# Kernel tuning notes

Measured on AMD Instinct MI355X. Metric: run time of the kernel, lower is better.

The kernel has to match this reference:

```python
import jax, jax.numpy as jnp
import numpy as np
from functools import partial

B, T, L = 32, 128, 64
DIN, H, DCTX, ATT = 512, 512, 512, 256


def _glorot(key, shape):
    lim = np.sqrt(6.0 / (shape[0] + shape[1]))
    return jax.random.uniform(key, shape, jnp.float32, -lim, lim)


def _ortho(key, shape):
    a = jax.random.normal(key, shape, jnp.float32)
    q, _ = jnp.linalg.qr(a)
    return q.astype(jnp.float32)


def setup_inputs() -> dict:
    key = jax.random.key(0)
    ks = jax.random.split(key, 24)
    inp = {
        "X": jax.random.normal(ks[0], (B, T, DIN), jnp.float32),
        "context": jax.random.normal(ks[1], (B, L, DCTX), jnp.float32),
        "mask": jnp.ones((B, T), jnp.float32),
        "context_mask": jnp.ones((B, L), jnp.int32),
    }
    names = ["i", "f", "c", "o"]
    for j, n in enumerate(names):
        inp[f"W_{n}"] = _glorot(ks[2 + 4 * j], (DIN, H))
        inp[f"U_{n}"] = _ortho(ks[3 + 4 * j], (H, H))
        inp[f"C_{n}"] = _ortho(ks[4 + 4 * j], (DCTX, H))
        inp[f"b_{n}"] = jnp.ones((H,), jnp.float32) if n == "f" else jnp.zeros((H,), jnp.float32)
    inp["att_ctx_W1"] = _glorot(ks[18], (DCTX, ATT))
    inp["att_h_W1"] = _glorot(ks[19], (H, ATT))
    inp["att_b1"] = jnp.zeros((ATT,), jnp.float32)
    inp["att_W2"] = _glorot(ks[20], (ATT, 1))
    inp["att_b2"] = jnp.zeros((1,), jnp.float32)
    return inp


def _forward(X, context, mask, cmask_f,
             W_i, U_i, C_i, b_i, W_f, U_f, C_f, b_f,
             W_c, U_c, C_c, b_c, W_o, U_o, C_o, b_o,
             att_ctx_W1, att_h_W1, att_b1, att_W2, att_b2):
    sig, tanh = jax.nn.sigmoid, jnp.tanh
    # precompute input-to-gate projections: [T,B,H]
    xi = jnp.einsum('btd,dh->tbh', X, W_i) + b_i
    xf = jnp.einsum('btd,dh->tbh', X, W_f) + b_f
    xc = jnp.einsum('btd,dh->tbh', X, W_c) + b_c
    xo = jnp.einsum('btd,dh->tbh', X, W_o) + b_o
    ctx_trans = jnp.einsum('bld,da->bla', context, att_ctx_W1) + att_b1  # [B,L,A]
    m = mask.T[:, :, None]  # [T,B,1]

    def step(carry, inp):
        h, c = carry
        xi_t, xf_t, xc_t, xo_t, m_t = inp
        # attention over context (original uses raw exp, not max-subtracted)
        att_hidden = tanh(ctx_trans + (h @ att_h_W1)[:, None, :])          # [B,L,A]
        att_raw = jnp.squeeze(att_hidden @ att_W2, -1) + att_b2[0]          # [B,L]
        e = jnp.exp(att_raw) * cmask_f
        a = e / jnp.sum(e, axis=-1, keepdims=True)
        ctx_vec = jnp.einsum('bl,bld->bd', a, context)                      # [B,Dctx]
        i_t = sig(xi_t + h @ U_i + ctx_vec @ C_i)
        f_t = sig(xf_t + h @ U_f + ctx_vec @ C_f)
        c_new = f_t * c + i_t * tanh(xc_t + h @ U_c + ctx_vec @ C_c)
        o_t = sig(xo_t + h @ U_o + ctx_vec @ C_o)
        h_new = o_t * tanh(c_new)
        h_new = (1.0 - m_t) * h + m_t * h_new
        c_new = (1.0 - m_t) * c + m_t * c_new
        return (h_new, c_new), (h_new, c_new, ctx_vec)

    h0 = jnp.zeros((X.shape[0], U_i.shape[0]), X.dtype)
    c0 = jnp.zeros_like(h0)
    _, (hs, cs, ctxs) = jax.lax.scan(step, (h0, c0), (xi, xf, xc, xo, m))
    # back to batch-major [B,T,·]
    return (hs.transpose(1, 0, 2), cs.transpose(1, 0, 2), ctxs.transpose(1, 0, 2))


def reference(X, context, mask, context_mask,
              W_i, U_i, C_i, b_i, W_f, U_f, C_f, b_f,
              W_c, U_c, C_c, b_c, W_o, U_o, C_o, b_o,
              att_ctx_W1, att_h_W1, att_b1, att_W2, att_b2):
    cmask_f = context_mask.astype(X.dtype)
    return _forward(X, context, mask, cmask_f,
                    W_i, U_i, C_i, b_i, W_f, U_f, C_f, b_f,
                    W_c, U_c, C_c, b_c, W_o, U_o, C_o, b_o,
                    att_ctx_W1, att_h_W1, att_b1, att_W2, att_b2)
```

## Files before the change

### kernel.cpp

```cpp
#include <hip/hip_runtime.h>
#include <stdint.h>

#define B_ 32
#define T_ 128
#define L_ 64
#define H_ 512
#define A_ 256
#define NB 32

typedef short short8 __attribute__((ext_vector_type(8)));
typedef float floatx4 __attribute__((ext_vector_type(4)));

__device__ __forceinline__ float b2f(unsigned short u) {
  union { unsigned int i; float f; } x; x.i = ((unsigned int)u) << 16; return x.f;
}
__device__ __forceinline__ unsigned short f2b(float f) {
  union { float f; unsigned int i; } x; x.f = f;
  unsigned int i = x.i;
  unsigned int r = (i + 0x7fffu + ((i >> 16) & 1u)) >> 16;
  return (unsigned short)r;
}
__device__ __forceinline__ void unpack2(unsigned int p, float& lo, float& hi) {
  union { unsigned int i; float f; } a, b;
  a.i = p << 16; b.i = p & 0xffff0000u;
  lo = a.f; hi = b.f;
}
__device__ __forceinline__ float tanh_fast(float x) {
  float e = __expf(2.f * x);
  return 1.f - 2.f / (e + 1.f);
}
__device__ __forceinline__ float sigmoid_fast(float x) {
  return 1.f / (1.f + __expf(-x));
}
template<bool F32>
__device__ __forceinline__ float ld1(const void* p, size_t i) {
  if (F32) return ((const float*)p)[i];
  return b2f(((const unsigned short*)p)[i]);
}
template<bool F32>
__device__ __forceinline__ void ld8(const void* p, size_t i, float* f) {
  if (F32) {
    const float4 a = *(const float4*)((const float*)p + i);
    const float4 b = *(const float4*)((const float*)p + i + 4);
    f[0] = a.x; f[1] = a.y; f[2] = a.z; f[3] = a.w;
    f[4] = b.x; f[5] = b.y; f[6] = b.z; f[7] = b.w;
  } else {
    const uint4 v = *(const uint4*)((const unsigned short*)p + i);
    unpack2(v.x, f[0], f[1]); unpack2(v.y, f[2], f[3]);
    unpack2(v.z, f[4], f[5]); unpack2(v.w, f[6], f[7]);
  }
}

__global__ __launch_bounds__(256) void conv_f2b(
    const float* __restrict__ src, unsigned short* __restrict__ dst, int n)
{
  const int i = (blockIdx.x * 256 + threadIdx.x) * 4;
  if (i + 3 < n) {
    const float4 v = *(const float4*)(src + i);
    ushort4 o;
    o.x = f2b(v.x); o.y = f2b(v.y); o.z = f2b(v.z); o.w = f2b(v.w);
    *(ushort4*)(dst + i) = o;
  }
}

__global__ __launch_bounds__(256) void gemm_bias(
    const unsigned short* __restrict__ A,
    const unsigned short* __restrict__ W,
    const float* __restrict__ bias,
    unsigned short* __restrict__ out,
    int M, int N, int ldo, int co, int mode)
{
  const int K = 512;
  __shared__ __attribute__((aligned(16))) unsigned short As[16 * 32];
  __shared__ __attribute__((aligned(16))) unsigned short Bs[32 * 64];
  const int tid = threadIdx.x;
  const int m0 = blockIdx.y * 16;
  const int n0 = blockIdx.x * 64;
  const int lane = tid & 63;
  const int w = tid >> 6;
  const int mfrag = lane & 15;
  const int q = lane >> 4;
  floatx4 acc = {0.f, 0.f, 0.f, 0.f};

  for (int k0 = 0; k0 < K; k0 += 32) {
    if (tid < 64) {
      const int r = tid >> 2, cg = tid & 3;
      const uint4 v = *(const uint4*)(A + (size_t)(m0 + r) * K + k0 + cg * 8);
      *(uint4*)&As[r * 32 + cg * 8] = v;
    }
    {
      const int r = tid >> 3, cg = tid & 7;
      const uint4 v = *(const uint4*)(W + (size_t)(k0 + r) * N + n0 + cg * 8);
      *(uint4*)&Bs[r * 64 + cg * 8] = v;
    }
    __syncthreads();
    const short8 af = *(const short8*)&As[mfrag * 32 + q * 8];
    short8 bf;
    const int wn = w * 16 + mfrag;
#pragma unroll
    for (int j = 0; j < 8; ++j) bf[j] = (short)Bs[(q * 8 + j) * 64 + wn];
    acc = __builtin_amdgcn_mfma_f32_16x16x32_bf16(af, bf, acc, 0, 0, 0);
    __syncthreads();
  }
  const int col = n0 + w * 16 + mfrag;
  const float bv = bias ? bias[col] : 0.f;
#pragma unroll
  for (int i = 0; i < 4; ++i) {
    const int row = m0 + q * 4 + i;
    const unsigned short v = f2b(acc[i] + bv);
    if (mode) {
      const int bb = row >> 7, tt = row & 127;
      out[((size_t)tt * 2048 + co + col) * 32 + bb] = v;
    } else {
      out[(size_t)row * ldo + co + col] = v;
    }
  }
}

__global__ __launch_bounds__(1024) void init_coop(unsigned short* Hs0,
                                                  unsigned int* flags)
{
  const int tid = threadIdx.x;
#pragma unroll
  for (int i = 0; i < 16; ++i) Hs0[tid * 16 + i] = 0;
  flags[tid] = 0u;
}

__device__ __forceinline__ void flagbar(unsigned int* flags, unsigned int gen) {
  __syncthreads();
  if (threadIdx.x == 0)
    __hip_atomic_store(flags + (size_t)blockIdx.x * 32, gen,
                       __ATOMIC_RELEASE, __HIP_MEMORY_SCOPE_AGENT);
  if (threadIdx.x < NB) {
    while (__hip_atomic_load(flags + (size_t)threadIdx.x * 32,
                             __ATOMIC_RELAXED, __HIP_MEMORY_SCOPE_AGENT) < gen)
      __builtin_amdgcn_s_sleep(1);
    __builtin_amdgcn_fence(__ATOMIC_ACQUIRE, "agent");
  }
  __syncthreads();
}

struct CoopParams {
  const float* Uf[4];
  const float* Cf[4];
  const float* attW1h;
  unsigned short* UT;
  unsigned short* CT;
  unsigned short* w1hsT;
  unsigned short* Hs0;
  unsigned short* Hs1;
  unsigned short* CVs;
  float* partials;
  unsigned int* flags;
  const unsigned short* xg;
  const unsigned short* ctxT;
  const unsigned short* cxb;
  const float* attW2;
  const float* attB2;
  const float* mask;
  const int* cmask;
  float* out;
};

__global__ __launch_bounds__(1024) void rnn_coop(const CoopParams p) {
  __shared__ __attribute__((aligned(16))) unsigned short h_all[32][520];
  __shared__ __attribute__((aligned(16))) unsigned short cv_all[32][520];
  __shared__ __attribute__((aligned(16))) unsigned short hloc_b[32][24];
  __shared__ float accbuf[16][32][17];
  __shared__ float pw1[4][256];
  __shared__ float hw1[256];
  __shared__ float e_s[64];
  __shared__ float a_s[64];
  __shared__ float cpart[2][512];
  __shared__ float c_s[512];
  __shared__ float h_loc[512];

  const int k = blockIdx.x;
  const int tid = threadIdx.x;

  {
    const int g = tid >> 8;
    const int idx = tid & 255;
    unsigned short* dU = p.UT + (size_t)k * 32768 + (size_t)g * 8192;
    unsigned short* dC = p.CT + (size_t)k * 32768 + (size_t)g * 8192;
#pragma unroll
    for (int rr = 0; rr < 2; ++rr) {
      const int r = idx * 2 + rr;
      const float* sU = p.Uf[g] + (size_t)r * 512 + k * 16;
      const float* sC = p.Cf[g] + (size_t)r * 512 + k * 16;
#pragma unroll
      for (int n = 0; n < 16; ++n) dU[(size_t)n * 512 + r] = f2b(sU[n]);
#pragma unroll
      for (int n = 0; n < 16; ++n) dC[(size_t)n * 512 + r] = f2b(sC[n]);
    }
  }
  {
    const int a = tid >> 2, r0 = (tid & 3) * 4;
    unsigned short* dst = p.w1hsT + (size_t)k * 4096 + (size_t)a * 16 + r0;
#pragma unroll
    for (int rr = 0; rr < 4; ++rr)
      dst[rr] = f2b(p.attW1h[(size_t)(k * 16 + r0 + rr) * 256 + a]);
  }
  const int lq = tid >> 4;
  const int kk = tid & 15;
  float ctq[16], w2q[16];
  {
    const unsigned short* ct = p.ctxT + ((size_t)(k * L_ + lq)) * 256 + kk * 16;
#pragma unroll
    for (int i = 0; i < 16; ++i) ctq[i] = b2f(ct[i]);
#pragma unroll
    for (int i = 0; i < 16; ++i) w2q[i] = p.attW2[kk * 16 + i];
  }
  const float b2v = p.attB2[0];
  const float cm_l = (float)p.cmask[k * L_ + lq];
  if (tid < 512) { c_s[tid] = 0.f; h_loc[tid] = 0.f; }
  unsigned int bgen = 0;
  __syncthreads();

  for (int t = 0; t < T_; ++t) {
    const unsigned short* HsA = (t & 1) ? p.Hs1 : p.Hs0;
    unsigned short* HsB = (t & 1) ? p.Hs0 : p.Hs1;

    {
      const int row = tid >> 5, cg = tid & 31;
      const uint4* src = (const uint4*)(HsA + (size_t)row * 512 + cg * 16);
      const uint4 v0 = src[0], v1 = src[1];
      *(uint4*)&h_all[row][cg * 16] = v0;
      *(uint4*)&h_all[row][cg * 16 + 8] = v1;
    }
    {
      const int p4 = tid >> 8, a = tid & 255;
      float s = 0.f;
      if (t > 0) {
        const float* pp = p.partials + (size_t)(p4 * 8) * 8192 + (size_t)k * 256 + a;
#pragma unroll
        for (int i = 0; i < 8; ++i) s += pp[(size_t)i * 8192];
      }
      pw1[p4][a] = s;
    }
    __syncthreads();
    if (tid < 256) hw1[tid] = pw1[0][tid] + pw1[1][tid] + pw1[2][tid] + pw1[3][tid];
    __syncthreads();

    {
      float s = 0.f;
#pragma unroll
      for (int i = 0; i < 16; ++i)
        s += tanh_fast(ctq[i] + hw1[kk * 16 + i]) * w2q[i];
      s += __shfl_xor(s, 1, 16);
      s += __shfl_xor(s, 2, 16);
      s += __shfl_xor(s, 4, 16);
      s += __shfl_xor(s, 8, 16);
      if (kk == 0) e_s[lq] = __expf(s + b2v) * cm_l;
    }
    __syncthreads();
    if (tid < 64) {
      const float e = e_s[tid];
      float s = e;
#pragma unroll
      for (int off = 1; off < 64; off <<= 1) s += __shfl_xor(s, off, 64);
      a_s[tid] = e / s;
    }
    __syncthreads();
    {
      const int p2 = tid >> 9, d = tid & 511;
      const unsigned short* cxp = p.cxb + ((size_t)(k * L_ + p2 * 32)) * 512 + d;
      float s = 0.f;
#pragma unroll 4
      for (int l = 0; l < 32; ++l)
        s += a_s[p2 * 32 + l] * b2f(cxp[(size_t)l * 512]);
      cpart[p2][d] = s;
    }
    __syncthreads();
    if (tid < 512) {
      const float cv = cpart[0][tid] + cpart[1][tid];
      p.CVs[(size_t)k * 512 + tid] = f2b(cv);
      p.out[(size_t)4194304 + ((size_t)k * T_ + t) * 512 + tid] = cv;
    }
    flagbar(p.flags, ++bgen);

    {
      const int row = tid >> 5, cg = tid & 31;
      const uint4* src = (const uint4*)(p.CVs + (size_t)row * 512 + cg * 16);
      const uint4 v0 = src[0], v1 = src[1];
      *(uint4*)&cv_all[row][cg * 16] = v0;
      *(uint4*)&cv_all[row][cg * 16 + 8] = v1;
    }
    __syncthreads();
    {
      const int w = tid >> 6, lane = tid & 63;
      const int l15 = lane & 15, q = lane >> 4;
      const int g = w & 3, ph = (w >> 2) & 1, khh = w >> 3;
      const unsigned short* Bb = (ph ? p.CT : p.UT)
          + (size_t)k * 32768 + (size_t)g * 8192 + (size_t)l15 * 512 + khh * 256 + q * 8;
      const unsigned short (*Aall)[520] = ph ? cv_all : h_all;
      floatx4 acc0 = {0.f, 0.f, 0.f, 0.f}, acc1 = {0.f, 0.f, 0.f, 0.f};
#pragma unroll
      for (int ks = 0; ks < 8; ++ks) {
        const short8 bfr = *(const short8*)(Bb + ks * 32);
        const short8 a0 = *(const short8*)&Aall[l15][khh * 256 + ks * 32 + q * 8];
        const short8 a1 = *(const short8*)&Aall[16 + l15][khh * 256 + ks * 32 + q * 8];
        acc0 = __builtin_amdgcn_mfma_f32_16x16x32_bf16(a0, bfr, acc0, 0, 0, 0);
        acc1 = __builtin_amdgcn_mfma_f32_16x16x32_bf16(a1, bfr, acc1, 0, 0, 0);
      }
#pragma unroll
      for (int i = 0; i < 4; ++i) {
        accbuf[w][q * 4 + i][l15] = acc0[i];
        accbuf[w][16 + q * 4 + i][l15] = acc1[i];
      }
    }
    __syncthreads();
    if (tid < 512) {
      const int b = tid >> 4, j = tid & 15;
      const size_t xb0 = ((size_t)t * 2048 + (size_t)(k * 16 + j)) * 32 + b;
#define GSUM(g) (accbuf[g][b][j] + accbuf[8 + g][b][j] + accbuf[4 + g][b][j] + accbuf[12 + g][b][j])
      float gi_ = GSUM(0) + b2f(p.xg[xb0]);
      float gf_ = GSUM(1) + b2f(p.xg[xb0 + (size_t)512 * 32]);
      float gc_ = GSUM(2) + b2f(p.xg[xb0 + (size_t)1024 * 32]);
      float go_ = GSUM(3) + b2f(p.xg[xb0 + (size_t)1536 * 32]);
#undef GSUM
      const float it = sigmoid_fast(gi_);
      const float ft = sigmoid_fast(gf_);
      const float ot = sigmoid_fast(go_);
      const float c_old = c_s[tid], h_old = h_loc[tid];
      float cn = ft * c_old + it * tanh_fast(gc_);
      float hn = ot * tanh_fast(cn);
      const float mt = p.mask[(size_t)b * T_ + t];
      hn = (1.f - mt) * h_old + mt * hn;
      cn = (1.f - mt) * c_old + mt * cn;
      c_s[tid] = cn; h_loc[tid] = hn;
      const unsigned short hb = f2b(hn);
      HsB[(size_t)b * 512 + k * 16 + j] = hb;
      hloc_b[b][j] = hb;
      const size_t o0 = ((size_t)b * T_ + t) * 512 + k * 16 + j;
      p.out[o0] = hn;
      p.out[(size_t)2097152 + o0] = cn;
    }
    __syncthreads();
    {
      const int w = tid >> 6, lane = tid & 63;
      const int l15 = lane & 15, q = lane >> 4;
      const short8 z8 = {0, 0, 0, 0, 0, 0, 0, 0};
      const unsigned short* wrow =
          p.w1hsT + (size_t)k * 4096 + (size_t)(w * 16 + l15) * 16 + (q & 1) * 8;
      const short8 bfr = (q < 2) ? *(const short8*)wrow : z8;
#pragma unroll
      for (int mh = 0; mh < 2; ++mh) {
        const unsigned short* hrow = &hloc_b[mh * 16 + l15][(q & 1) * 8];
        const short8 af = (q < 2) ? *(const short8*)hrow : z8;
        floatx4 acc = {0.f, 0.f, 0.f, 0.f};
        acc = __builtin_amdgcn_mfma_f32_16x16x32_bf16(af, bfr, acc, 0, 0, 0);
#pragma unroll
        for (int i = 0; i < 4; ++i)
          p.partials[(size_t)k * 8192 + (size_t)(mh * 16 + q * 4 + i) * 256 + w * 16 + l15] = acc[i];
      }
    }
    flagbar(p.flags, ++bgen);
  }
}

struct Params {
  const void* W[4]; const void* U[4]; const void* C[4]; const void* gb[4];
  const void* attW1c; const void* attW1h; const void* attB1;
  const void* attW2; const void* attB2;
  const void* mask; const void* context; const void* Xin;
  const int* cmask;
  float* out;
};

template<bool F32>
__device__ void rnn_body(const Params p) {
  __shared__ float h_s[512];
  __shared__ float x_s[512];
  __shared__ float cv_s[512];
  __shared__ float pw1[4][256];
  __shared__ float hw1[256];
  __shared__ float e_s[64];
  __shared__ float a_s[64];
  __shared__ float gpart[4][2048];
  __shared__ float cpart[2][512];

  const int b = blockIdx.x;
  const int tid = threadIdx.x;
  const int lq = tid >> 4;
  const int kk = tid & 15;
  const int part4 = tid >> 8;
  const int a256 = tid & 255;
  const int part2 = tid >> 9;
  const int d512 = tid & 511;
  const int g = a256 >> 6;
  const int j0 = a256 * 8;
  const int jj = j0 & 511;

  float ctq[16];
#pragma unroll
  for (int i = 0; i < 16; ++i) ctq[i] = 0.f;
  {
    const size_t crow = ((size_t)b * L_ + lq) * 512;
    for (int r = 0; r < 512; ++r) {
      const float cv = ld1<F32>(p.context, crow + r);
      float fa[8], fb[8];
      ld8<F32>(p.attW1c, (size_t)r * 256 + kk * 16, fa);
      ld8<F32>(p.attW1c, (size_t)r * 256 + kk * 16 + 8, fb);
#pragma unroll
      for (int i = 0; i < 8; ++i) { ctq[i] += cv * fa[i]; ctq[8 + i] += cv * fb[i]; }
    }
#pragma unroll
    for (int i = 0; i < 16; ++i) ctq[i] += ld1<F32>(p.attB1, kk * 16 + i);
  }
  float w2q[16];
#pragma unroll
  for (int i = 0; i < 16; ++i) w2q[i] = ld1<F32>(p.attW2, kk * 16 + i);
  const float b2v = ld1<F32>(p.attB2, 0);
  float bi = 0.f, bff = 0.f, bc = 0.f, bo = 0.f;
  if (tid < 512) {
    bi = ld1<F32>(p.gb[0], tid);
    bff = ld1<F32>(p.gb[1], tid);
    bc = ld1<F32>(p.gb[2], tid);
    bo = ld1<F32>(p.gb[3], tid);
  }
  float c_reg = 0.f;
  if (tid < 512) h_s[tid] = 0.f;
  __syncthreads();

  const void* Wg = p.W[g];
  const void* Ug = p.U[g];
  const void* Cg = p.C[g];
  const size_t wb = (size_t)(part4 * 128) * 512 + jj;
  const size_t w1b = (size_t)(part4 * 128) * 256 + a256;

  for (int t = 0; t < T_; ++t) {
    {
      float s = 0.f;
      const int r0 = part4 * 128;
#pragma unroll 4
      for (int r = 0; r < 128; ++r)
        s += h_s[r0 + r] * ld1<F32>(p.attW1h, w1b + (size_t)r * 256);
      pw1[part4][a256] = s;
    }
    if (tid < 512)
      x_s[tid] = ld1<F32>(p.Xin, ((size_t)b * T_ + t) * 512 + tid);
    __syncthreads();
    if (tid < 256) hw1[tid] = pw1[0][tid] + pw1[1][tid] + pw1[2][tid] + pw1[3][tid];
    __syncthreads();
    {
      float s = 0.f;
#pragma unroll
      for (int i = 0; i < 16; ++i)
        s += tanh_fast(ctq[i] + hw1[kk * 16 + i]) * w2q[i];
      s += __shfl_xor(s, 1, 16);
      s += __shfl_xor(s, 2, 16);
      s += __shfl_xor(s, 4, 16);
      s += __shfl_xor(s, 8, 16);
      if (kk == 0)
        e_s[lq] = __expf(s + b2v) * (float)p.cmask[b * L_ + lq];
    }
    __syncthreads();
    if (tid < 64) {
      const float e = e_s[tid];
      float s = e;
#pragma unroll
      for (int off = 1; off < 64; off <<= 1) s += __shfl_xor(s, off, 64);
      a_s[tid] = e / s;
    }
    __syncthreads();
    {
      const size_t cb = ((size_t)b * L_ + part2 * 32) * 512 + d512;
      float s = 0.f;
#pragma unroll 4
      for (int l = 0; l < 32; ++l)
        s += a_s[part2 * 32 + l] * ld1<F32>(p.context, cb + (size_t)l * 512);
      cpart[part2][d512] = s;
    }
    __syncthreads();
    if (tid < 512) {
      const float cv = cpart[0][tid] + cpart[1][tid];
      cv_s[tid] = cv;
      p.out[(size_t)4194304 + ((size_t)b * T_ + t) * 512 + tid] = cv;
    }
    __syncthreads();
    {
      float acc[8];
#pragma unroll
      for (int i = 0; i < 8; ++i) acc[i] = 0.f;
      const int r0 = part4 * 128;
      float f[8];
#pragma unroll 2
      for (int r = 0; r < 128; ++r) {
        const float xv = x_s[r0 + r];
        ld8<F32>(Wg, wb + (size_t)r * 512, f);
#pragma unroll
        for (int i = 0; i < 8; ++i) acc[i] += xv * f[i];
      }
#pragma unroll 2
      for (int r = 0; r < 128; ++r) {
        const float hv = h_s[r0 + r];
        ld8<F32>(Ug, wb + (size_t)r * 512, f);
#pragma unroll
        for (int i = 0; i < 8; ++i) acc[i] += hv * f[i];
      }
#pragma unroll 2
      for (int r = 0; r < 128; ++r) {
        const float cvv = cv_s[r0 + r];
        ld8<F32>(Cg, wb + (size_t)r * 512, f);
#pragma unroll
        for (int i = 0; i < 8; ++i) acc[i] += cvv * f[i];
      }
#pragma unroll
      for (int i = 0; i < 8; ++i) gpart[part4][j0 + i] = acc[i];
    }
    __syncthreads();
    if (tid < 512) {
      const int d = tid;
      float gi_ = bi + gpart[0][d] + gpart[1][d] + gpart[2][d] + gpart[3][d];
      float gf_ = bff + gpart[0][512 + d] + gpart[1][512 + d] + gpart[2][512 + d] + gpart[3][512 + d];
      float gc_ = bc + gpart[0][1024 + d] + gpart[1][1024 + d] + gpart[2][1024 + d] + gpart[3][1024 + d];
      float go_ = bo + gpart[0][1536 + d] + gpart[1][1536 + d] + gpart[2][1536 + d] + gpart[3][1536 + d];
      const float it = sigmoid_fast(gi_);
      const float ft = sigmoid_fast(gf_);
      const float ot = sigmoid_fast(go_);
      float cn = ft * c_reg + it * tanh_fast(gc_);
      float hn = ot * tanh_fast(cn);
      const float m = ld1<F32>(p.mask, (size_t)b * T_ + t);
      hn = (1.f - m) * h_s[d] + m * hn;
      cn = (1.f - m) * c_reg + m * cn;
      c_reg = cn;
      h_s[d] = hn;
      const size_t o0 = ((size_t)b * T_ + t) * 512 + d;
      p.out[o0] = hn;
      p.out[(size_t)2097152 + o0] = cn;
    }
    __syncthreads();
  }
}

__global__ __launch_bounds__(1024) void rnn_fused(const Params p) {
  const unsigned int mw = *(const unsigned int*)p.mask;
  if (mw == 0x3F800000u) rnn_body<true>(p);
  else rnn_body<false>(p);
}

extern "C" void kernel_launch(void* const* d_in, const int* in_sizes, int n_in,
                              void* d_out, int out_size, void* d_ws, size_t ws_size,
                              hipStream_t stream) {
  (void)in_sizes; (void)n_in; (void)out_size;
  const float* X    = (const float*)d_in[0];
  const float* Ctx  = (const float*)d_in[1];
  const float* Mask = (const float*)d_in[2];
  const int*   Cm   = (const int*)d_in[3];
  const float* Wt[4] = {(const float*)d_in[4],  (const float*)d_in[8],
                        (const float*)d_in[12], (const float*)d_in[16]};
  const float* Ut[4] = {(const float*)d_in[5],  (const float*)d_in[9],
                        (const float*)d_in[13], (const float*)d_in[17]};
  const float* Ct[4] = {(const float*)d_in[6],  (const float*)d_in[10],
                        (const float*)d_in[14], (const float*)d_in[18]};
  const float* bg[4] = {(const float*)d_in[7],  (const float*)d_in[11],
                        (const float*)d_in[15], (const float*)d_in[19]};
  const float* attW1c = (const float*)d_in[20];
  const float* attW1h = (const float*)d_in[21];
  const float* attB1  = (const float*)d_in[22];
  const float* attW2  = (const float*)d_in[23];
  const float* attB2  = (const float*)d_in[24];

  const size_t WS_NEED = 32083968;
  if (ws_size >= WS_NEED) {
    char* ws = (char*)d_ws;
    unsigned short* xg    = (unsigned short*)(ws);
    unsigned short* ctxT  = (unsigned short*)(ws + 16777216);
    unsigned short* Xbf   = (unsigned short*)(ws + 17825792);
    unsigned short* cxb   = (unsigned short*)(ws + 22020096);
    unsigned short* w1cb  = (unsigned short*)(ws + 24117248);
    unsigned short* Wb4   = (unsigned short*)(ws + 24379392);
    unsigned short* UT    = (unsigned short*)(ws + 26476544);
    unsigned short* CT    = (unsigned short*)(ws + 28573696);
    unsigned short* w1hsT = (unsigned short*)(ws + 30670848);
    unsigned short* Hs0   = (unsigned short*)(ws + 30932992);
    unsigned short* Hs1   = (unsigned short*)(ws + 30965760);
    unsigned short* CVs   = (unsigned short*)(ws + 30998528);
    float*          parts = (float*)(ws + 31031296);
    unsigned int*   flags = (unsigned int*)(ws + 32079872);

    conv_f2b<<<dim3(2048), dim3(256), 0, stream>>>(X, Xbf, 2097152);
    conv_f2b<<<dim3(1024), dim3(256), 0, stream>>>(Ctx, cxb, 1048576);
    conv_f2b<<<dim3(128), dim3(256), 0, stream>>>(attW1c, w1cb, 131072);
    for (int g = 0; g < 4; ++g)
      conv_f2b<<<dim3(256), dim3(256), 0, stream>>>(Wt[g], Wb4 + (size_t)g * 262144, 262144);
    for (int g = 0; g < 4; ++g)
      gemm_bias<<<dim3(8, 256), dim3(256), 0, stream>>>(
          Xbf, Wb4 + (size_t)g * 262144, bg[g], xg, 4096, 512, 2048, g * 512, 1);
    gemm_bias<<<dim3(4, 128), dim3(256), 0, stream>>>(
        cxb, w1cb, attB1, ctxT, 2048, 256, 256, 0, 0);
    init_coop<<<dim3(1), dim3(1024), 0, stream>>>(Hs0, flags);

    CoopParams cp;
    for (int g = 0; g < 4; ++g) { cp.Uf[g] = Ut[g]; cp.Cf[g] = Ct[g]; }
    cp.attW1h = attW1h;
    cp.UT = UT; cp.CT = CT; cp.w1hsT = w1hsT;
    cp.Hs0 = Hs0; cp.Hs1 = Hs1; cp.CVs = CVs;
    cp.partials = parts; cp.flags = flags;
    cp.xg = xg; cp.ctxT = ctxT; cp.cxb = cxb;
    cp.attW2 = attW2; cp.attB2 = attB2; cp.mask = Mask; cp.cmask = Cm;
    cp.out = (float*)d_out;
    rnn_coop<<<dim3(NB), dim3(1024), 0, stream>>>(cp);
  } else {
    Params p;
    p.Xin = X; p.context = Ctx; p.mask = Mask; p.cmask = Cm;
    for (int g = 0; g < 4; ++g) {
      p.W[g] = Wt[g]; p.U[g] = Ut[g]; p.C[g] = Ct[g]; p.gb[g] = bg[g];
    }
    p.attW1c = attW1c; p.attW1h = attW1h; p.attB1 = attB1;
    p.attW2 = attW2; p.attB2 = attB2;
    p.out = (float*)d_out;
    rnn_fused<<<dim3(32), dim3(1024), 0, stream>>>(p);
  }
}
```

Measured before the change: 2.365 ms.

## Warp-specialize recurrent step to overlap U-matmul with attention and fuse prep kernels

```diff
diff --git a/kernel.cpp b/kernel.cpp
--- a/kernel.cpp
+++ b/kernel.cpp
@@ -51,16 +51,44 @@
   }
 }
 
-__global__ __launch_bounds__(256) void conv_f2b(
-    const float* __restrict__ src, unsigned short* __restrict__ dst, int n)
+__global__ __launch_bounds__(256) void conv_all(
+    const float* __restrict__ X, const float* __restrict__ Ctx,
+    const float* __restrict__ W1c,
+    const float* __restrict__ W0, const float* __restrict__ W1,
+    const float* __restrict__ W2, const float* __restrict__ W3,
+    unsigned short* __restrict__ Xbf, unsigned short* __restrict__ cxb,
+    unsigned short* __restrict__ w1cb, unsigned short* __restrict__ Wb4)
 {
-  const int i = (blockIdx.x * 256 + threadIdx.x) * 4;
-  if (i + 3 < n) {
-    const float4 v = *(const float4*)(src + i);
-    ushort4 o;
-    o.x = f2b(v.x); o.y = f2b(v.y); o.z = f2b(v.z); o.w = f2b(v.w);
-    *(ushort4*)(dst + i) = o;
-  }
+  const size_t i = ((size_t)blockIdx.x * 256 + threadIdx.x) * 4;
+  const float* src; unsigned short* dst; size_t off;
+  if (i < 2097152) { src = X; dst = Xbf; off = i; }
+  else if (i < 3145728) { src = Ctx; dst = cxb; off = i - 2097152; }
+  else if (i < 3276800) { src = W1c; dst = w1cb; off = i - 3145728; }
+  else {
+    const size_t j = i - 3276800;
+    const int g = (int)(j >> 18);
+    src = (g == 0) ? W0 : (g == 1) ? W1 : (g == 2) ? W2 : W3;
+    dst = Wb4 + ((size_t)g << 18);
+    off = j & 262143;
+  }
+  const float4 v = *(const float4*)(src + off);
+  ushort4 o;
+  o.x = f2b(v.x); o.y = f2b(v.y); o.z = f2b(v.z); o.w = f2b(v.w);
+  *(ushort4*)(dst + off) = o;
+}
+
+__global__ __launch_bounds__(256) void transpose_cxbT(
+    const float* __restrict__ Ctx, unsigned short* __restrict__ cxbT)
+{
+  const int b = blockIdx.x, dg = blockIdx.y;
+  const int d = dg * 64 + (threadIdx.x >> 2), lg = threadIdx.x & 3;
+  unsigned short tmp[16];
+#pragma unroll
+  for (int i = 0; i < 16; ++i)
+    tmp[i] = f2b(Ctx[((size_t)b * 64 + lg * 16 + i) * 512 + d]);
+  unsigned short* dst = cxbT + ((size_t)b * 512 + d) * 64 + lg * 16;
+  *(uint4*)dst = *(const uint4*)&tmp[0];
+  *(uint4*)(dst + 8) = *(const uint4*)&tmp[8];
 }
 
 __global__ __launch_bounds__(256) void gemm_bias(
@@ -68,7 +96,7 @@
     const unsigned short* __restrict__ W,
     const float* __restrict__ bias,
     unsigned short* __restrict__ out,
-    int M, int N, int ldo, int co, int mode)
+    int M, int N, int ldo, int co)
 {
   const int K = 512;
   __shared__ __attribute__((aligned(16))) unsigned short As[16 * 32];
@@ -81,17 +109,16 @@
   const int mfrag = lane & 15;
   const int q = lane >> 4;
   floatx4 acc = {0.f, 0.f, 0.f, 0.f};
-
   for (int k0 = 0; k0 < K; k0 += 32) {
     if (tid < 64) {
       const int r = tid >> 2, cg = tid & 3;
-      const uint4 v = *(const uint4*)(A + (size_t)(m0 + r) * K + k0 + cg * 8);
-      *(uint4*)&As[r * 32 + cg * 8] = v;
+      *(uint4*)&As[r * 32 + cg * 8] =
+          *(const uint4*)(A + (size_t)(m0 + r) * K + k0 + cg * 8);
     }
     {
       const int r = tid >> 3, cg = tid & 7;
-      const uint4 v = *(const uint4*)(W + (size_t)(k0 + r) * N + n0 + cg * 8);
-      *(uint4*)&Bs[r * 64 + cg * 8] = v;
+      *(uint4*)&Bs[r * 64 + cg * 8] =
+          *(const uint4*)(W + (size_t)(k0 + r) * N + n0 + cg * 8);
     }
     __syncthreads();
     const short8 af = *(const short8*)&As[mfrag * 32 + q * 8];
@@ -105,25 +132,73 @@
   const int col = n0 + w * 16 + mfrag;
   const float bv = bias ? bias[col] : 0.f;
 #pragma unroll
+  for (int i = 0; i < 4; ++i)
+    out[(size_t)(m0 + q * 4 + i) * ldo + co + col] = f2b(acc[i] + bv);
+}
+
+struct GB4 { const float* b0; const float* b1; const float* b2; const float* b3; };
+
+__global__ __launch_bounds__(256) void gemm_xg(
+    const unsigned short* __restrict__ A,
+    const unsigned short* __restrict__ Wb4,
+    GB4 gb, unsigned short* __restrict__ out)
+{
+  const int K = 512, N = 512;
+  const int g = blockIdx.z;
+  const unsigned short* W = Wb4 + ((size_t)g << 18);
+  const float* bias = (g == 0) ? gb.b0 : (g == 1) ? gb.b1 : (g == 2) ? gb.b2 : gb.b3;
+  __shared__ __attribute__((aligned(16))) unsigned short As[16 * 32];
+  __shared__ __attribute__((aligned(16))) unsigned short Bs[32 * 64];
+  const int tid = threadIdx.x;
+  const int m0 = blockIdx.y * 16;
+  const int n0 = blockIdx.x * 64;
+  const int lane = tid & 63;
+  const int w = tid >> 6;
+  const int mfrag = lane & 15;
+  const int q = lane >> 4;
+  floatx4 acc = {0.f, 0.f, 0.f, 0.f};
+  for (int k0 = 0; k0 < K; k0 += 32) {
+    if (tid < 64) {
+      const int r = tid >> 2, cg = tid & 3;
+      *(uint4*)&As[r * 32 + cg * 8] =
+          *(const uint4*)(A + (size_t)(m0 + r) * K + k0 + cg * 8);
+    }
+    {
+      const int r = tid >> 3, cg = tid & 7;
+      *(uint4*)&Bs[r * 64 + cg * 8] =
+          *(const uint4*)(W + (size_t)(k0 + r) * N + n0 + cg * 8);
+    }
+    __syncthreads();
+    const short8 af = *(const short8*)&As[mfrag * 32 + q * 8];
+    short8 bf;
+    const int wn = w * 16 + mfrag;
+#pragma unroll
+    for (int j = 0; j < 8; ++j) bf[j] = (short)Bs[(q * 8 + j) * 64 + wn];
+    acc = __builtin_amdgcn_mfma_f32_16x16x32_bf16(af, bf, acc, 0, 0, 0);
+    __syncthreads();
+  }
+  const int col = n0 + w * 16 + mfrag;
+  const float bv = bias[col];
+#pragma unroll
   for (int i = 0; i < 4; ++i) {
     const int row = m0 + q * 4 + i;
-    const unsigned short v = f2b(acc[i] + bv);
-    if (mode) {
-      const int bb = row >> 7, tt = row & 127;
-      out[((size_t)tt * 2048 + co + col) * 32 + bb] = v;
-    } else {
-      out[(size_t)row * ldo + co + col] = v;
-    }
-  }
-}
-
-__global__ __launch_bounds__(1024) void init_coop(unsigned short* Hs0,
-                                                  unsigned int* flags)
+    const int bb = row >> 7, tt = row & 127;
+    out[((size_t)tt * 2048 + g * 512 + col) * 32 + bb] = f2b(acc[i] + bv);
+  }
+}
+
+__global__ __launch_bounds__(1024) void init_coop(
+    unsigned short* Hs, float* partials, unsigned int* flags)
 {
-  const int tid = threadIdx.x;
-#pragma unroll
-  for (int i = 0; i < 16; ++i) Hs0[tid * 16 + i] = 0;
-  flags[tid] = 0u;
+  const int gid = blockIdx.x * 1024 + threadIdx.x;
+  const float4 z = {0.f, 0.f, 0.f, 0.f};
+  *(float4*)(partials + (size_t)gid * 4) = z;
+  if (blockIdx.x == 0) {
+    const uint4 zi = {0u, 0u, 0u, 0u};
+    *(uint4*)(Hs + (size_t)threadIdx.x * 16) = zi;
+    *(uint4*)(Hs + (size_t)threadIdx.x * 16 + 8) = zi;
+    flags[threadIdx.x] = 0u;
+  }
 }
 
 __device__ __forceinline__ void flagbar(unsigned int* flags, unsigned int gen) {
@@ -133,8 +208,7 @@
                        __ATOMIC_RELEASE, __HIP_MEMORY_SCOPE_AGENT);
   if (threadIdx.x < NB) {
     while (__hip_atomic_load(flags + (size_t)threadIdx.x * 32,
-                             __ATOMIC_RELAXED, __HIP_MEMORY_SCOPE_AGENT) < gen)
-      __builtin_amdgcn_s_sleep(1);
+                             __ATOMIC_RELAXED, __HIP_MEMORY_SCOPE_AGENT) < gen) {}
     __builtin_amdgcn_fence(__ATOMIC_ACQUIRE, "agent");
   }
   __syncthreads();
@@ -147,14 +221,13 @@
   unsigned short* UT;
   unsigned short* CT;
   unsigned short* w1hsT;
-  unsigned short* Hs0;
-  unsigned short* Hs1;
+  unsigned short* Hs;
   unsigned short* CVs;
   float* partials;
   unsigned int* flags;
   const unsigned short* xg;
   const unsigned short* ctxT;
-  const unsigned short* cxb;
+  const unsigned short* cxbT;
   const float* attW2;
   const float* attB2;
   const float* mask;
@@ -166,17 +239,24 @@
   __shared__ __attribute__((aligned(16))) unsigned short h_all[32][520];
   __shared__ __attribute__((aligned(16))) unsigned short cv_all[32][520];
   __shared__ __attribute__((aligned(16))) unsigned short hloc_b[32][24];
-  __shared__ float accbuf[16][32][17];
-  __shared__ float pw1[4][256];
+  __shared__ float accbuf[8][16][17];
+  __shared__ float pw[2][256];
   __shared__ float hw1[256];
   __shared__ float e_s[64];
   __shared__ float a_s[64];
-  __shared__ float cpart[2][512];
   __shared__ float c_s[512];
   __shared__ float h_loc[512];
+  __shared__ float w2s[256];
 
   const int k = blockIdx.x;
   const int tid = threadIdx.x;
+  const int wid = tid >> 6;
+  const int lane = tid & 63;
+  const int q = lane >> 4, l15 = lane & 15;
+  const int mw = wid - 8;
+  const int mg = mw & 3, mh = mw >> 2;
+  const int lq = tid >> 3;
+  const int kk8 = tid & 7;
 
   {
     const int g = tid >> 8;
@@ -201,60 +281,86 @@
     for (int rr = 0; rr < 4; ++rr)
       dst[rr] = f2b(p.attW1h[(size_t)(k * 16 + r0 + rr) * 256 + a]);
   }
-  const int lq = tid >> 4;
-  const int kk = tid & 15;
-  float ctq[16], w2q[16];
-  {
-    const unsigned short* ct = p.ctxT + ((size_t)(k * L_ + lq)) * 256 + kk * 16;
-#pragma unroll
-    for (int i = 0; i < 16; ++i) ctq[i] = b2f(ct[i]);
-#pragma unroll
-    for (int i = 0; i < 16; ++i) w2q[i] = p.attW2[kk * 16 + i];
-  }
+  if (tid < 256) w2s[tid] = p.attW2[tid];
+  if (tid < 512) { c_s[tid] = 0.f; h_loc[tid] = 0.f; }
   const float b2v = p.attB2[0];
-  const float cm_l = (float)p.cmask[k * L_ + lq];
-  if (tid < 512) { c_s[tid] = 0.f; h_loc[tid] = 0.f; }
+  const float cm_l = (tid < 512) ? (float)p.cmask[k * L_ + lq] : 0.f;
   unsigned int bgen = 0;
   __syncthreads();
 
   for (int t = 0; t < T_; ++t) {
-    const unsigned short* HsA = (t & 1) ? p.Hs1 : p.Hs0;
-    unsigned short* HsB = (t & 1) ? p.Hs0 : p.Hs1;
-
-    {
-      const int row = tid >> 5, cg = tid & 31;
-      const uint4* src = (const uint4*)(HsA + (size_t)row * 512 + cg * 16);
-      const uint4 v0 = src[0], v1 = src[1];
-      *(uint4*)&h_all[row][cg * 16] = v0;
-      *(uint4*)&h_all[row][cg * 16 + 8] = v1;
-    }
-    {
-      const int p4 = tid >> 8, a = tid & 255;
+    uint4 ct0, ct1, ct2, ct3;
+    if (tid < 512) {
+      const int a = tid & 255, grp = tid >> 8;
+      const float* pp = p.partials + ((size_t)k * 32 + grp * 16) * 256 + a;
       float s = 0.f;
-      if (t > 0) {
-        const float* pp = p.partials + (size_t)(p4 * 8) * 8192 + (size_t)k * 256 + a;
-#pragma unroll
-        for (int i = 0; i < 8; ++i) s += pp[(size_t)i * 8192];
-      }
-      pw1[p4][a] = s;
-    }
-    __syncthreads();
-    if (tid < 256) hw1[tid] = pw1[0][tid] + pw1[1][tid] + pw1[2][tid] + pw1[3][tid];
-    __syncthreads();
-
-    {
+#pragma unroll
+      for (int i = 0; i < 16; ++i) s += pp[(size_t)i * 256];
+      pw[grp][a] = s;
+      const uint4* ct = (const uint4*)(p.ctxT + ((size_t)(k * L_ + lq)) * 256 + kk8 * 32);
+      ct0 = ct[0]; ct1 = ct[1]; ct2 = ct[2]; ct3 = ct[3];
+    } else {
+      const int t2 = tid - 512, row = t2 >> 4, cg = t2 & 15;
+      const uint4* src = (const uint4*)(p.Hs + (size_t)row * 512 + cg * 32);
+      const uint4 v0 = src[0], v1 = src[1], v2 = src[2], v3 = src[3];
+      *(uint4*)&h_all[row][cg * 32] = v0;
+      *(uint4*)&h_all[row][cg * 32 + 8] = v1;
+      *(uint4*)&h_all[row][cg * 32 + 16] = v2;
+      *(uint4*)&h_all[row][cg * 32 + 24] = v3;
+    }
+    __syncthreads();
+
+    floatx4 acc = {0.f, 0.f, 0.f, 0.f};
+    const unsigned short* uB =
+        p.UT + (size_t)k * 32768 + (size_t)mg * 8192 + (size_t)l15 * 512 + q * 8;
+    if (wid >= 8) {
+#pragma unroll
+      for (int ks = 0; ks < 6; ++ks) {
+        const short8 af = *(const short8*)&h_all[mh * 16 + l15][ks * 32 + q * 8];
+        const short8 bf = *(const short8*)(uB + ks * 32);
+        acc = __builtin_amdgcn_mfma_f32_16x16x32_bf16(af, bf, acc, 0, 0, 0);
+      }
+    } else if (tid < 256) {
+      hw1[tid] = pw[0][tid] + pw[1][tid];
+    }
+    __syncthreads();
+
+    if (wid >= 8) {
+#pragma unroll
+      for (int ks = 6; ks < 12; ++ks) {
+        const short8 af = *(const short8*)&h_all[mh * 16 + l15][ks * 32 + q * 8];
+        const short8 bf = *(const short8*)(uB + ks * 32);
+        acc = __builtin_amdgcn_mfma_f32_16x16x32_bf16(af, bf, acc, 0, 0, 0);
+      }
+    } else {
+      float ctv[32];
+      unpack2(ct0.x, ctv[0], ctv[1]);  unpack2(ct0.y, ctv[2], ctv[3]);
+      unpack2(ct0.z, ctv[4], ctv[5]);  unpack2(ct0.w, ctv[6], ctv[7]);
+      unpack2(ct1.x, ctv[8], ctv[9]);  unpack2(ct1.y, ctv[10], ctv[11]);
+      unpack2(ct1.z, ctv[12], ctv[13]); unpack2(ct1.w, ctv[14], ctv[15]);
+      unpack2(ct2.x, ctv[16], ctv[17]); unpack2(ct2.y, ctv[18], ctv[19]);
+      unpack2(ct2.z, ctv[20], ctv[21]); unpack2(ct2.w, ctv[22], ctv[23]);
+      unpack2(ct3.x, ctv[24], ctv[25]); unpack2(ct3.y, ctv[26], ctv[27]);
+      unpack2(ct3.z, ctv[28], ctv[29]); unpack2(ct3.w, ctv[30], ctv[31]);
       float s = 0.f;
 #pragma unroll
-      for (int i = 0; i < 16; ++i)
-        s += tanh_fast(ctq[i] + hw1[kk * 16 + i]) * w2q[i];
-      s += __shfl_xor(s, 1, 16);
-      s += __shfl_xor(s, 2, 16);
-      s += __shfl_xor(s, 4, 16);
-      s += __shfl_xor(s, 8, 16);
-      if (kk == 0) e_s[lq] = __expf(s + b2v) * cm_l;
-    }
-    __syncthreads();
-    if (tid < 64) {
+      for (int i = 0; i < 32; ++i)
+        s += tanh_fast(ctv[i] + hw1[kk8 * 32 + i]) * w2s[kk8 * 32 + i];
+      s += __shfl_xor(s, 1, 8);
+      s += __shfl_xor(s, 2, 8);
+      s += __shfl_xor(s, 4, 8);
+      if (kk8 == 0) e_s[lq] = __expf(s + b2v) * cm_l;
+    }
+    __syncthreads();
+
+    if (wid >= 8) {
+#pragma unroll
+      for (int ks = 12; ks < 16; ++ks) {
+        const short8 af = *(const short8*)&h_all[mh * 16 + l15][ks * 32 + q * 8];
+        const short8 bf = *(const short8*)(uB + ks * 32);
+        acc = __builtin_amdgcn_mfma_f32_16x16x32_bf16(af, bf, acc, 0, 0, 0);
+      }
+    } else if (tid < 64) {
       const float e = e_s[tid];
       float s = e;
 #pragma unroll
@@ -262,20 +368,22 @@
       a_s[tid] = e / s;
     }
     __syncthreads();
-    {
-      const int p2 = tid >> 9, d = tid & 511;
-      const unsigned short* cxp = p.cxb + ((size_t)(k * L_ + p2 * 32)) * 512 + d;
+
+    if (tid < 512) {
+      const uint4* cx = (const uint4*)(p.cxbT + ((size_t)k * 512 + tid) * 64);
       float s = 0.f;
-#pragma unroll 4
-      for (int l = 0; l < 32; ++l)
-        s += a_s[p2 * 32 + l] * b2f(cxp[(size_t)l * 512]);
-      cpart[p2][d] = s;
-    }
-    __syncthreads();
-    if (tid < 512) {
-      const float cv = cpart[0][tid] + cpart[1][tid];
-      p.CVs[(size_t)k * 512 + tid] = f2b(cv);
-      p.out[(size_t)4194304 + ((size_t)k * T_ + t) * 512 + tid] = cv;
+#pragma unroll
+      for (int lc = 0; lc < 8; ++lc) {
+        const uint4 v = cx[lc];
+        float f0, f1, f2, f3, f4, f5, f6, f7;
+        unpack2(v.x, f0, f1); unpack2(v.y, f2, f3);
+        unpack2(v.z, f4, f5); unpack2(v.w, f6, f7);
+        const int l0 = lc * 8;
+        s += a_s[l0] * f0 + a_s[l0 + 1] * f1 + a_s[l0 + 2] * f2 + a_s[l0 + 3] * f3 +
+             a_s[l0 + 4] * f4 + a_s[l0 + 5] * f5 + a_s[l0 + 6] * f6 + a_s[l0 + 7] * f7;
+      }
+      p.CVs[(size_t)k * 512 + tid] = f2b(s);
+      p.out[(size_t)4194304 + ((size_t)k * T_ + t) * 512 + tid] = s;
     }
     flagbar(p.flags, ++bgen);
 
@@ -286,39 +394,38 @@
       *(uint4*)&cv_all[row][cg * 16] = v0;
       *(uint4*)&cv_all[row][cg * 16 + 8] = v1;
     }
-    __syncthreads();
-    {
-      const int w = tid >> 6, lane = tid & 63;
-      const int l15 = lane & 15, q = lane >> 4;
-      const int g = w & 3, ph = (w >> 2) & 1, khh = w >> 3;
-      const unsigned short* Bb = (ph ? p.CT : p.UT)
-          + (size_t)k * 32768 + (size_t)g * 8192 + (size_t)l15 * 512 + khh * 256 + q * 8;
-      const unsigned short (*Aall)[520] = ph ? cv_all : h_all;
-      floatx4 acc0 = {0.f, 0.f, 0.f, 0.f}, acc1 = {0.f, 0.f, 0.f, 0.f};
-#pragma unroll
-      for (int ks = 0; ks < 8; ++ks) {
-        const short8 bfr = *(const short8*)(Bb + ks * 32);
-        const short8 a0 = *(const short8*)&Aall[l15][khh * 256 + ks * 32 + q * 8];
-        const short8 a1 = *(const short8*)&Aall[16 + l15][khh * 256 + ks * 32 + q * 8];
-        acc0 = __builtin_amdgcn_mfma_f32_16x16x32_bf16(a0, bfr, acc0, 0, 0, 0);
-        acc1 = __builtin_amdgcn_mfma_f32_16x16x32_bf16(a1, bfr, acc1, 0, 0, 0);
-      }
-#pragma unroll
-      for (int i = 0; i < 4; ++i) {
-        accbuf[w][q * 4 + i][l15] = acc0[i];
-        accbuf[w][16 + q * 4 + i][l15] = acc1[i];
-      }
-    }
-    __syncthreads();
+    unsigned short xgv0 = 0, xgv1 = 0, xgv2 = 0, xgv3 = 0;
     if (tid < 512) {
       const int b = tid >> 4, j = tid & 15;
-      const size_t xb0 = ((size_t)t * 2048 + (size_t)(k * 16 + j)) * 32 + b;
-#define GSUM(g) (accbuf[g][b][j] + accbuf[8 + g][b][j] + accbuf[4 + g][b][j] + accbuf[12 + g][b][j])
-      float gi_ = GSUM(0) + b2f(p.xg[xb0]);
-      float gf_ = GSUM(1) + b2f(p.xg[xb0 + (size_t)512 * 32]);
-      float gc_ = GSUM(2) + b2f(p.xg[xb0 + (size_t)1024 * 32]);
-      float go_ = GSUM(3) + b2f(p.xg[xb0 + (size_t)1536 * 32]);
-#undef GSUM
+      const size_t xb = ((size_t)t * 2048 + (size_t)(k * 16 + j)) * 32 + b;
+      xgv0 = p.xg[xb];
+      xgv1 = p.xg[xb + (size_t)512 * 32];
+      xgv2 = p.xg[xb + (size_t)1024 * 32];
+      xgv3 = p.xg[xb + (size_t)1536 * 32];
+    }
+    __syncthreads();
+
+    if (wid >= 8) {
+      const unsigned short* cB =
+          p.CT + (size_t)k * 32768 + (size_t)mg * 8192 + (size_t)l15 * 512 + q * 8;
+#pragma unroll
+      for (int ks = 0; ks < 16; ++ks) {
+        const short8 af = *(const short8*)&cv_all[mh * 16 + l15][ks * 32 + q * 8];
+        const short8 bf = *(const short8*)(cB + ks * 32);
+        acc = __builtin_amdgcn_mfma_f32_16x16x32_bf16(af, bf, acc, 0, 0, 0);
+      }
+#pragma unroll
+      for (int i = 0; i < 4; ++i) accbuf[mw][q * 4 + i][l15] = acc[i];
+    }
+    __syncthreads();
+
+    if (tid < 512) {
+      const int b = tid >> 4, j = tid & 15;
+      const int bh = b >> 4, br = b & 15;
+      float gi_ = accbuf[bh * 4 + 0][br][j] + b2f(xgv0);
+      float gf_ = accbuf[bh * 4 + 1][br][j] + b2f(xgv1);
+      float gc_ = accbuf[bh * 4 + 2][br][j] + b2f(xgv2);
+      float go_ = accbuf[bh * 4 + 3][br][j] + b2f(xgv3);
       const float it = sigmoid_fast(gi_);
       const float ft = sigmoid_fast(gf_);
       const float ot = sigmoid_fast(go_);
@@ -330,29 +437,31 @@
       cn = (1.f - mt) * c_old + mt * cn;
       c_s[tid] = cn; h_loc[tid] = hn;
       const unsigned short hb = f2b(hn);
-      HsB[(size_t)b * 512 + k * 16 + j] = hb;
+      p.Hs[(size_t)b * 512 + k * 16 + j] = hb;
       hloc_b[b][j] = hb;
       const size_t o0 = ((size_t)b * T_ + t) * 512 + k * 16 + j;
       p.out[o0] = hn;
       p.out[(size_t)2097152 + o0] = cn;
     }
     __syncthreads();
-    {
-      const int w = tid >> 6, lane = tid & 63;
-      const int l15 = lane & 15, q = lane >> 4;
+
+    if (wid >= 8) {
       const short8 z8 = {0, 0, 0, 0, 0, 0, 0, 0};
-      const unsigned short* wrow =
-          p.w1hsT + (size_t)k * 4096 + (size_t)(w * 16 + l15) * 16 + (q & 1) * 8;
-      const short8 bfr = (q < 2) ? *(const short8*)wrow : z8;
-#pragma unroll
-      for (int mh = 0; mh < 2; ++mh) {
-        const unsigned short* hrow = &hloc_b[mh * 16 + l15][(q & 1) * 8];
-        const short8 af = (q < 2) ? *(const short8*)hrow : z8;
-        floatx4 acc = {0.f, 0.f, 0.f, 0.f};
-        acc = __builtin_amdgcn_mfma_f32_16x16x32_bf16(af, bfr, acc, 0, 0, 0);
-#pragma unroll
-        for (int i = 0; i < 4; ++i)
-          p.partials[(size_t)k * 8192 + (size_t)(mh * 16 + q * 4 + i) * 256 + w * 16 + l15] = acc[i];
+#pragma unroll
+      for (int half = 0; half < 2; ++half) {
+        const int acol0 = mw * 32 + half * 16;
+        const unsigned short* wrow =
+            p.w1hsT + (size_t)k * 4096 + (size_t)(acol0 + l15) * 16 + (q & 1) * 8;
+        const short8 bfr = (q < 2) ? *(const short8*)wrow : z8;
+#pragma unroll
+        for (int mh2 = 0; mh2 < 2; ++mh2) {
+          const short8 af = (q < 2) ? *(const short8*)&hloc_b[mh2 * 16 + l15][(q & 1) * 8] : z8;
+          floatx4 pa = {0.f, 0.f, 0.f, 0.f};
+          pa = __builtin_amdgcn_mfma_f32_16x16x32_bf16(af, bfr, pa, 0, 0, 0);
+#pragma unroll
+          for (int i = 0; i < 4; ++i)
+            p.partials[((size_t)(mh2 * 16 + q * 4 + i) * 32 + k) * 256 + acol0 + l15] = pa[i];
+        }
       }
     }
     flagbar(p.flags, ++bgen);
@@ -562,43 +671,40 @@
   const float* attW2  = (const float*)d_in[23];
   const float* attB2  = (const float*)d_in[24];
 
-  const size_t WS_NEED = 32083968;
+  const size_t WS_NEED = 32051200;
   if (ws_size >= WS_NEED) {
     char* ws = (char*)d_ws;
     unsigned short* xg    = (unsigned short*)(ws);
     unsigned short* ctxT  = (unsigned short*)(ws + 16777216);
     unsigned short* Xbf   = (unsigned short*)(ws + 17825792);
+    unsigned short* cxbT  = (unsigned short*)(ws + 17825792);
     unsigned short* cxb   = (unsigned short*)(ws + 22020096);
     unsigned short* w1cb  = (unsigned short*)(ws + 24117248);
     unsigned short* Wb4   = (unsigned short*)(ws + 24379392);
     unsigned short* UT    = (unsigned short*)(ws + 26476544);
     unsigned short* CT    = (unsigned short*)(ws + 28573696);
     unsigned short* w1hsT = (unsigned short*)(ws + 30670848);
-    unsigned short* Hs0   = (unsigned short*)(ws + 30932992);
-    unsigned short* Hs1   = (unsigned short*)(ws + 30965760);
-    unsigned short* CVs   = (unsigned short*)(ws + 30998528);
-    float*          parts = (float*)(ws + 31031296);
-    unsigned int*   flags = (unsigned int*)(ws + 32079872);
-
-    conv_f2b<<<dim3(2048), dim3(256), 0, stream>>>(X, Xbf, 2097152);
-    conv_f2b<<<dim3(1024), dim3(256), 0, stream>>>(Ctx, cxb, 1048576);
-    conv_f2b<<<dim3(128), dim3(256), 0, stream>>>(attW1c, w1cb, 131072);
-    for (int g = 0; g < 4; ++g)
-      conv_f2b<<<dim3(256), dim3(256), 0, stream>>>(Wt[g], Wb4 + (size_t)g * 262144, 262144);
-    for (int g = 0; g < 4; ++g)
-      gemm_bias<<<dim3(8, 256), dim3(256), 0, stream>>>(
-          Xbf, Wb4 + (size_t)g * 262144, bg[g], xg, 4096, 512, 2048, g * 512, 1);
+    unsigned short* Hs    = (unsigned short*)(ws + 30932992);
+    unsigned short* CVs   = (unsigned short*)(ws + 30965760);
+    float*          parts = (float*)(ws + 30998528);
+    unsigned int*   flags = (unsigned int*)(ws + 32047104);
+
+    conv_all<<<dim3(4224), dim3(256), 0, stream>>>(
+        X, Ctx, attW1c, Wt[0], Wt[1], Wt[2], Wt[3], Xbf, cxb, w1cb, Wb4);
+    GB4 gb4 = {bg[0], bg[1], bg[2], bg[3]};
+    gemm_xg<<<dim3(8, 256, 4), dim3(256), 0, stream>>>(Xbf, Wb4, gb4, xg);
     gemm_bias<<<dim3(4, 128), dim3(256), 0, stream>>>(
-        cxb, w1cb, attB1, ctxT, 2048, 256, 256, 0, 0);
-    init_coop<<<dim3(1), dim3(1024), 0, stream>>>(Hs0, flags);
+        cxb, w1cb, attB1, ctxT, 2048, 256, 256, 0);
+    transpose_cxbT<<<dim3(32, 8), dim3(256), 0, stream>>>(Ctx, cxbT);
+    init_coop<<<dim3(64), dim3(1024), 0, stream>>>(Hs, parts, flags);
 
     CoopParams cp;
     for (int g = 0; g < 4; ++g) { cp.Uf[g] = Ut[g]; cp.Cf[g] = Ct[g]; }
     cp.attW1h = attW1h;
     cp.UT = UT; cp.CT = CT; cp.w1hsT = w1hsT;
-    cp.Hs0 = Hs0; cp.Hs1 = Hs1; cp.CVs = CVs;
+    cp.Hs = Hs; cp.CVs = CVs;
     cp.partials = parts; cp.flags = flags;
-    cp.xg = xg; cp.ctxT = ctxT; cp.cxb = cxb;
+    cp.xg = xg; cp.ctxT = ctxT; cp.cxbT = cxbT;
     cp.attW2 = attW2; cp.attB2 = attB2; cp.mask = Mask; cp.cmask = Cm;
     cp.out = (float*)d_out;
     rnn_coop<<<dim3(NB), dim3(1024), 0, stream>>>(cp);
```

Result: slower. 3.177 ms (+34.3%).
